# Kernel tuning notes

Hardware: AMD Instinct MI355X
Metric: run time of the kernel (lower is better)

## Reference

```python
import jax, jax.numpy as jnp
import numpy as np

N = 100000  # number of nodes
SELF_LOOP_W = 2.0  # improved=True in PyG GCNConv


def gcn_conv(x, edge_index, W, b):
    # x: [N, Fin], edge_index: [2, E] (row=src, col=dst), W: [Fin, Fout], b: [Fout]
    src, dst = edge_index[0], edge_index[1]
    h = x @ W  # [N, Fout]
    # degree with improved self-loops (weight 2.0)
    ones = jnp.ones(src.shape, dtype=h.dtype)
    deg = jax.ops.segment_sum(ones, dst, num_segments=N) + SELF_LOOP_W
    dinv = jnp.where(deg > 0, jax.lax.rsqrt(deg), 0.0)
    norm = dinv[src] * dinv[dst]  # [E]
    agg = jax.ops.segment_sum(h[src] * norm[:, None], dst, num_segments=N)
    # self-loop contribution: weight 2.0, norm = dinv_i * 2 * dinv_i
    agg = agg + h * (SELF_LOOP_W * dinv * dinv)[:, None]
    return agg + b


def setup_inputs() -> dict:
    key = jax.random.key(0)
    ks = jax.random.split(key, 6)
    x = jax.random.normal(ks[0], (N, 64), dtype=jnp.float32)
    edge_index = jax.random.randint(ks[1], (2, 1600000), 0, N, dtype=jnp.int64)
    W1 = jax.random.normal(ks[2], (64, 64), dtype=jnp.float32) * 0.1
    b1 = jax.random.normal(ks[3], (64,), dtype=jnp.float32) * 0.1
    W2 = jax.random.normal(ks[4], (64, 32), dtype=jnp.float32) * 0.1
    b2 = jax.random.normal(ks[5], (32,), dtype=jnp.float32) * 0.1
    return {"x": x, "edge_index": edge_index, "W1": W1, "b1": b1, "W2": W2, "b2": b2}


def reference(x, edge_index, W1, b1, W2, b2):
    h1 = jax.nn.relu(gcn_conv(x, edge_index, W1, b1))
    feature_map = h1
    out = gcn_conv(h1, edge_index, W2, b2)
    return (out, feature_map)
```

## Files before the change

### kernel.cpp

```cpp
#include <hip/hip_runtime.h>

#define N_NODES 100000
#define E_EDGES 1600000

#define BSHIFT 7
#define BSIZE 128
#define NBUCK ((N_NODES + BSIZE - 1) / BSIZE)
#define STAGE_TPB 512
#define STAGE_EPT 8
#define STAGE_CHUNK (STAGE_TPB * STAGE_EPT)
#define NREP 2
#define BUCKET_CAP 4096
#define CSR_STRIDE (BUCKET_CAP + 512)

typedef __attribute__((ext_vector_type(8))) short short8;
typedef __attribute__((ext_vector_type(4))) float float4v;
typedef __attribute__((ext_vector_type(2))) float float2v;
typedef __attribute__((ext_vector_type(4))) int int4v;
typedef __attribute__((ext_vector_type(4))) unsigned uint4v;

__device__ inline unsigned short f2bf(float f) {
    union { float f; unsigned u; } t; t.f = f;
    unsigned r = (t.u + 0x7fffu + ((t.u >> 16) & 1u)) >> 16;
    return (unsigned short)r;
}
__device__ inline float bf2f(unsigned short h) {
    union { unsigned u; float f; } t; t.u = ((unsigned)h) << 16; return t.f;
}
__device__ inline unsigned pack_bf16x2(float a, float b) {
    return (unsigned)f2bf(a) | ((unsigned)f2bf(b) << 16);
}
__device__ inline float bf_lo(unsigned u) { union { unsigned u; float f; } t; t.u = u << 16; return t.f; }
__device__ inline float bf_hi(unsigned u) { union { unsigned u; float f; } t; t.u = u & 0xffff0000u; return t.f; }

__device__ inline float2v bfpair(unsigned u) {
    float2v r;
    r[0] = bf_lo(u);
    r[1] = bf_hi(u);
    return r;
}
__device__ inline float2v pk_add(float2v a, float2v b) {
    float2v d;
    asm("v_pk_add_f32 %0, %1, %2" : "=v"(d) : "v"(a), "v"(b));
    return d;
}

__global__ void cursor_init_kernel(int* __restrict__ gcursor,
                                   unsigned* __restrict__ HS1, unsigned* __restrict__ HS2) {
    int b = blockIdx.x * blockDim.x + threadIdx.x;
    if (b < NBUCK) gcursor[b] = b * BUCKET_CAP;
    if (b < 32) HS1[(size_t)N_NODES * 32 + b] = 0u;
    if (b < 16) HS2[(size_t)N_NODES * 16 + b] = 0u;
}

__global__ void __launch_bounds__(STAGE_TPB) stage_kernel(
    const int* __restrict__ src, const int* __restrict__ dst,
    int* __restrict__ gcursor, unsigned* __restrict__ staged, int E) {
    __shared__ int hist[NREP][NBUCK];
    __shared__ int dbase[NBUCK];
    __shared__ int scanw[1024];
    __shared__ unsigned lrec[STAGE_CHUNK];
    __shared__ int laddr[STAGE_CHUNK];
    const int tid = threadIdx.x;
    const int rep = (tid >> 8) & (NREP - 1);
    const int e0 = blockIdx.x * STAGE_CHUNK;
    for (int i = tid; i < NREP * NBUCK; i += STAGE_TPB) ((int*)hist)[i] = 0;
    scanw[tid] = 0; scanw[tid + 512] = 0;
    __syncthreads();
    int d[STAGE_EPT], s[STAGE_EPT];
#pragma unroll
    for (int k = 0; k < STAGE_EPT / 4; ++k) {
        int e = e0 + (k * STAGE_TPB + tid) * 4;
        if (e < E) {
            int4v sv = __builtin_nontemporal_load((const int4v*)(src + e));
            int4v dv = __builtin_nontemporal_load((const int4v*)(dst + e));
#pragma unroll
            for (int i = 0; i < 4; ++i) {
                s[4 * k + i] = sv[i];
                d[4 * k + i] = dv[i];
                atomicAdd(&hist[rep][dv[i] >> BSHIFT], 1);
            }
        } else {
#pragma unroll
            for (int i = 0; i < 4; ++i) d[4 * k + i] = -1;
        }
    }
    __syncthreads();
    for (int i = tid; i < NBUCK; i += STAGE_TPB) scanw[i] = hist[0][i] + hist[1][i];
    if (tid + 512 < NBUCK) scanw[tid + 512] = hist[0][tid + 512] + hist[1][tid + 512];
    __syncthreads();
    for (int off = 1; off < 1024; off <<= 1) {
        int v0 = (tid >= off) ? scanw[tid - off] : 0;
        int v1 = (tid + 512 >= off) ? scanw[tid + 512 - off] : 0;
        __syncthreads();
        scanw[tid] += v0;
        scanw[tid + 512] += v1;
        __syncthreads();
    }
    for (int i = tid; i < NBUCK; i += STAGE_TPB) {
        int h0 = hist[0][i], h1 = hist[1][i];
        int t = h0 + h1;
        int excl = scanw[i] - t;
        if (t > 0) {
            int g = atomicAdd(&gcursor[i], t);
            dbase[i] = g - excl;
        }
        hist[0][i] = excl;
        hist[1][i] = excl + h0;
    }
    __syncthreads();
#pragma unroll
    for (int k = 0; k < STAGE_EPT; ++k) {
        if (d[k] >= 0) {
            int b = d[k] >> BSHIFT;
            int slot = atomicAdd(&hist[rep][b], 1);
            lrec[slot] = (unsigned)s[k] | ((unsigned)(d[k] & (BSIZE - 1)) << 17);
            laddr[slot] = dbase[b] + slot;
        }
    }
    __syncthreads();
    const int total = min(STAGE_CHUNK, E - e0);
    for (int i = tid; i < total; i += STAGE_TPB) {
        int a = laddr[i];
        if ((unsigned)a < (unsigned)(NBUCK * BUCKET_CAP))
            staged[a] = lrec[i];
    }
}

__global__ void bucket_csr_kernel(const unsigned* __restrict__ staged,
                                  const int* __restrict__ gcursor,
                                  int4v* __restrict__ meta, float* __restrict__ dinv,
                                  int* __restrict__ csrc, int n) {
    __shared__ int ldeg[BSIZE];
    __shared__ int laex[BSIZE];
    __shared__ int lscan[BSIZE];
    __shared__ int lcnt[BSIZE];
    __shared__ int h2[32];
    __shared__ int c2[32];
    __shared__ unsigned lrec[BUCKET_CAP];
    __shared__ int lsrc[BUCKET_CAP + 512];
    __shared__ int ltot;
    const int b = blockIdx.x;
    const int node0 = b * BSIZE;
    const int nn = min(BSIZE, n - node0);
    const int tid = threadIdx.x;
    if (tid < BSIZE) { ldeg[tid] = 0; lcnt[tid] = 0; }
    if (tid < 32) { h2[tid] = 0; c2[tid] = 0; }
    __syncthreads();
    const int ebase = b * CSR_STRIDE;
    int ecnt = gcursor[b] - b * BUCKET_CAP;
    if (ecnt > BUCKET_CAP) ecnt = BUCKET_CAP;
    const int sbase = b * BUCKET_CAP;
    for (int i = tid; i < ecnt; i += 256) {
        unsigned r = staged[sbase + i];
        lrec[i] = r;
        atomicAdd(&ldeg[(r >> 17) & (BSIZE - 1)], 1);
    }
    __syncthreads();
    int mydeg = (tid < BSIZE) ? ldeg[tid] : 0;
    int adeg = (mydeg + 3) & ~3;
    if (tid < BSIZE) lscan[tid] = adeg;
    __syncthreads();
    for (int off = 1; off < BSIZE; off <<= 1) {
        int v = 0;
        if (tid < BSIZE && tid >= off) v = lscan[tid - off];
        __syncthreads();
        if (tid < BSIZE) lscan[tid] += v;
        __syncthreads();
    }
    const int bin = min(adeg >> 2, 31);
    float mydinv = 0.0f;
    if (tid < BSIZE) {
        int aex = lscan[tid] - adeg;
        laex[tid] = aex;
        if (tid == BSIZE - 1) ltot = lscan[tid];
        if (tid < nn) {
            mydinv = rsqrtf((float)mydeg + 2.0f);
            dinv[node0 + tid] = mydinv;
            for (int k = mydeg; k < adeg; ++k) lsrc[aex + k] = N_NODES;
            atomicAdd(&h2[bin], 1);
        }
    }
    __syncthreads();
    if (tid == 0) {
        int acc = 0;
        for (int k = 0; k < 32; ++k) { int v = h2[k]; h2[k] = acc; acc += v; }
    }
    __syncthreads();
    if (tid < nn) {
        int pos = h2[bin] + atomicAdd(&c2[bin], 1);
        union { float f; int i; } dv; dv.f = mydinv;
        meta[node0 + pos] = (int4v){ebase + laex[tid], mydeg, node0 + tid, dv.i};
    }
    for (int i = tid; i < ecnt; i += 256) {
        unsigned r = lrec[i];
        int dl = (int)((r >> 17) & (BSIZE - 1));
        int sv = (int)(r & 0x1FFFFu);
        int pos = laex[dl] + atomicAdd(&lcnt[dl], 1);
        if (pos < BUCKET_CAP + 512) lsrc[pos] = sv;
    }
    __syncthreads();
    const int tot = ltot;
    for (int i = tid; i < tot; i += 256)
        csrc[ebase + i] = lsrc[i];
}

template <int FOUT>
__global__ void __launch_bounds__(256) linear_mfma_kernel(
    const float* __restrict__ X, const float* __restrict__ W,
    const float* __restrict__ dinv, unsigned* __restrict__ HS, int n) {
    constexpr int NT = FOUT / 16;
    constexpr int ROWU = NT * 8;
    const int NTILES_M = n / 16;
    const int lane = threadIdx.x & 63;
    const int gwave = blockIdx.x * 4 + (threadIdx.x >> 6);
    const int nwaves = gridDim.x * 4;
    const int m = lane & 15;
    const int q = lane >> 4;

    short8 Bhi[2][NT], Blo[2][NT];
#pragma unroll
    for (int ks = 0; ks < 2; ++ks)
#pragma unroll
        for (int nt = 0; nt < NT; ++nt) {
            short8 bh, bl;
#pragma unroll
            for (int j = 0; j < 8; ++j) {
                int k = ks * 32 + q * 8 + j;
                float wv = W[k * FOUT + nt * 16 + m];
                unsigned short h = f2bf(wv);
                bh[j] = (short)h;
                bl[j] = (short)f2bf(wv - bf2f(h));
            }
            Bhi[ks][nt] = bh;
            Blo[ks][nt] = bl;
        }

    for (int tile = gwave; tile < NTILES_M; tile += nwaves) {
        const int row0 = tile * 16;
        float4v C[NT];
#pragma unroll
        for (int nt = 0; nt < NT; ++nt) C[nt] = (float4v){0.f, 0.f, 0.f, 0.f};
#pragma unroll
        for (int ks = 0; ks < 2; ++ks) {
            const float* xp = X + (size_t)(row0 + m) * 64 + ks * 32 + q * 8;
            float4v x0 = __builtin_nontemporal_load((const float4v*)xp);
            float4v x1 = __builtin_nontemporal_load((const float4v*)(xp + 4));
            short8 Ahi, Alo;
#pragma unroll
            for (int j = 0; j < 4; ++j) {
                unsigned short h0 = f2bf(x0[j]);
                Ahi[j] = (short)h0;
                Alo[j] = (short)f2bf(x0[j] - bf2f(h0));
                unsigned short h1 = f2bf(x1[j]);
                Ahi[4 + j] = (short)h1;
                Alo[4 + j] = (short)f2bf(x1[j] - bf2f(h1));
            }
#pragma unroll
            for (int nt = 0; nt < NT; ++nt) {
                C[nt] = __builtin_amdgcn_mfma_f32_16x16x32_bf16(Ahi, Bhi[ks][nt], C[nt], 0, 0, 0);
                C[nt] = __builtin_amdgcn_mfma_f32_16x16x32_bf16(Alo, Bhi[ks][nt], C[nt], 0, 0, 0);
                C[nt] = __builtin_amdgcn_mfma_f32_16x16x32_bf16(Ahi, Blo[ks][nt], C[nt], 0, 0, 0);
            }
        }
#pragma unroll
        for (int ch = 0; ch < NT / 2; ++ch) {
#pragma unroll
            for (int reg = 0; reg < 4; ++reg) {
                int r = row0 + q * 4 + reg;
                float di = dinv[r];
                unsigned u = pack_bf16x2(C[2 * ch][reg] * di, C[2 * ch + 1][reg] * di);
                __builtin_nontemporal_store(u, HS + (size_t)r * ROWU + ch * 16 + m);
            }
        }
    }
}

template <int ROWU, bool RELU>
__global__ void __launch_bounds__(256) gather_vec_kernel(
    const int4v* __restrict__ meta, const int* __restrict__ csrc,
    const unsigned* __restrict__ HS, const float* __restrict__ bias,
    float* __restrict__ OUT, int n) {
    constexpr int G = ROWU / 4;
    constexpr int NPB = 256 / G;
    constexpr int FOUT = ROWU * 2;
    const int gslot = blockIdx.x * NPB + (int)(threadIdx.x / G);
    const int t = threadIdx.x % G;
    if (gslot >= n) return;
    const int4v mi = meta[gslot];
    const int start = mi[0];
    const int deg = mi[1];
    const int node = mi[2];
    union { int i; float f; } dv; dv.i = mi[3];
    const float dd = dv.f;
    const int pend = start + ((deg + 3) & ~3);
    const unsigned* __restrict__ HSt = HS + 4 * t;
    const uint4v own = *(const uint4v*)(HS + (size_t)node * ROWU + 4 * t);
    float2v acc[4];
#pragma unroll
    for (int k = 0; k < 4; ++k) {
        float2v o = bfpair(own[k]);
        acc[k][0] = 2.0f * o[0];
        acc[k][1] = 2.0f * o[1];
    }
    int j = start;
    for (; j + 8 <= pend; j += 8) {
        int4v s0 = __builtin_nontemporal_load((const int4v*)(csrc + j));
        int4v s1 = __builtin_nontemporal_load((const int4v*)(csrc + j + 4));
        uint4v u0 = *(const uint4v*)(HSt + (size_t)s0[0] * ROWU);
        uint4v u1 = *(const uint4v*)(HSt + (size_t)s0[1] * ROWU);
        uint4v u2 = *(const uint4v*)(HSt + (size_t)s0[2] * ROWU);
        uint4v u3 = *(const uint4v*)(HSt + (size_t)s0[3] * ROWU);
        uint4v u4 = *(const uint4v*)(HSt + (size_t)s1[0] * ROWU);
        uint4v u5 = *(const uint4v*)(HSt + (size_t)s1[1] * ROWU);
        uint4v u6 = *(const uint4v*)(HSt + (size_t)s1[2] * ROWU);
        uint4v u7 = *(const uint4v*)(HSt + (size_t)s1[3] * ROWU);
#pragma unroll
        for (int k = 0; k < 4; ++k) {
            float2v p01 = pk_add(bfpair(u0[k]), bfpair(u1[k]));
            float2v p23 = pk_add(bfpair(u2[k]), bfpair(u3[k]));
            float2v p45 = pk_add(bfpair(u4[k]), bfpair(u5[k]));
            float2v p67 = pk_add(bfpair(u6[k]), bfpair(u7[k]));
            acc[k] = pk_add(acc[k], pk_add(pk_add(p01, p23), pk_add(p45, p67)));
        }
    }
    if (j < pend) {
        int4v s0 = __builtin_nontemporal_load((const int4v*)(csrc + j));
        uint4v u0 = *(const uint4v*)(HSt + (size_t)s0[0] * ROWU);
        uint4v u1 = *(const uint4v*)(HSt + (size_t)s0[1] * ROWU);
        uint4v u2 = *(const uint4v*)(HSt + (size_t)s0[2] * ROWU);
        uint4v u3 = *(const uint4v*)(HSt + (size_t)s0[3] * ROWU);
#pragma unroll
        for (int k = 0; k < 4; ++k) {
            float2v p01 = pk_add(bfpair(u0[k]), bfpair(u1[k]));
            float2v p23 = pk_add(bfpair(u2[k]), bfpair(u3[k]));
            acc[k] = pk_add(acc[k], pk_add(p01, p23));
        }
    }
    const int ch = t >> 2;
    const int c0 = (4 * t) & 15;
    const float4v blv = *(const float4v*)(bias + 32 * ch + c0);
    const float4v bhv = *(const float4v*)(bias + 32 * ch + 16 + c0);
    float4v olo, ohi;
#pragma unroll
    for (int k = 0; k < 4; ++k) {
        float o0 = acc[k][0] * dd + blv[k];
        float o1 = acc[k][1] * dd + bhv[k];
        if (RELU) { o0 = fmaxf(o0, 0.0f); o1 = fmaxf(o1, 0.0f); }
        olo[k] = o0;
        ohi[k] = o1;
    }
    float* op = OUT + (size_t)node * FOUT + 32 * ch + c0;
    __builtin_nontemporal_store(olo, (float4v*)op);
    __builtin_nontemporal_store(ohi, (float4v*)(op + 16));
}

extern "C" void kernel_launch(void* const* d_in, const int* in_sizes, int n_in,
                              void* d_out, int out_size, void* d_ws, size_t ws_size,
                              hipStream_t stream) {
    const float* x  = (const float*)d_in[0];
    const int*   ei = (const int*)d_in[1];
    const float* W1 = (const float*)d_in[2];
    const float* b1 = (const float*)d_in[3];
    const float* W2 = (const float*)d_in[4];
    const float* b2 = (const float*)d_in[5];

    const int* srcp = ei;
    const int* dstp = ei + E_EDGES;

    float* out = (float*)d_out;
    float* fm  = (float*)d_out + N_NODES * 32;

    char* w = (char*)d_ws;
    auto alloc = [&w](size_t bytes) -> void* {
        uintptr_t p = ((uintptr_t)w + 255) & ~(uintptr_t)255;
        w = (char*)(p + bytes);
        return (void*)p;
    };
    int*      gcursor  = (int*)alloc(sizeof(int) * NBUCK);
    int4v*    meta     = (int4v*)alloc(sizeof(int4v) * N_NODES);
    float*    dinv     = (float*)alloc(sizeof(float) * N_NODES);
    int*      csrc     = (int*)alloc(sizeof(int) * (size_t)NBUCK * CSR_STRIDE);
    unsigned* staged   = (unsigned*)alloc(sizeof(unsigned) * (size_t)NBUCK * BUCKET_CAP);
    unsigned* HS1      = (unsigned*)alloc(sizeof(unsigned) * (size_t)(N_NODES + 1) * 32);
    unsigned* HS2      = (unsigned*)alloc(sizeof(unsigned) * (size_t)(N_NODES + 1) * 16);

    cursor_init_kernel<<<(NBUCK + 255) / 256, 256, 0, stream>>>(gcursor, HS1, HS2);
    stage_kernel<<<(E_EDGES + STAGE_CHUNK - 1) / STAGE_CHUNK, STAGE_TPB, 0, stream>>>(
        srcp, dstp, gcursor, staged, E_EDGES);
    bucket_csr_kernel<<<NBUCK, 256, 0, stream>>>(staged, gcursor, meta, dinv, csrc, N_NODES);

    linear_mfma_kernel<64><<<512, 256, 0, stream>>>(x, W1, dinv, HS1, N_NODES);
    gather_vec_kernel<32, true><<<(N_NODES + 31) / 32, 256, 0, stream>>>(
        meta, csrc, HS1, b1, fm, N_NODES);

    linear_mfma_kernel<32><<<512, 256, 0, stream>>>(fm, W2, dinv, HS2, N_NODES);
    gather_vec_kernel<16, false><<<(N_NODES + 63) / 64, 256, 0, stream>>>(
        meta, csrc, HS2, b2, out, N_NODES);
}
```

Before: 197.8 us.

## Run first-layer GEMM concurrently with edge staging and fuse dinv scaling into CSR build

Extra blocks are appended to the edge staging kernel that compute the unscaled x@W1 product into a new fp32 buffer P, so the GEMM overlaps with the atomic-heavy bucketing work. The bucket CSR kernel then reads P, scales each row by its freshly computed dinv, packs to bf16 and writes HS1, which removes the separate first linear kernel launch. The cost is an extra round trip of a 100000x64 fp32 intermediate through memory and more shared/register pressure in the merged kernel, and the GEMM blocks share the stage kernel's large LDS footprint, which may limit occupancy.

```diff
diff --git a/kernel.cpp b/kernel.cpp
--- a/kernel.cpp
+++ b/kernel.cpp
@@ -9,6 +9,8 @@
 #define STAGE_TPB 512
 #define STAGE_EPT 8
 #define STAGE_CHUNK (STAGE_TPB * STAGE_EPT)
+#define NSTAGE ((E_EDGES + STAGE_CHUNK - 1) / STAGE_CHUNK)
+#define NGEMM 121
 #define NREP 2
 #define BUCKET_CAP 4096
 #define CSR_STRIDE (BUCKET_CAP + 512)
@@ -53,88 +55,152 @@
     if (b < 16) HS2[(size_t)N_NODES * 16 + b] = 0u;
 }
 
-__global__ void __launch_bounds__(STAGE_TPB) stage_kernel(
+__global__ void __launch_bounds__(STAGE_TPB) stage_gemm_kernel(
     const int* __restrict__ src, const int* __restrict__ dst,
-    int* __restrict__ gcursor, unsigned* __restrict__ staged, int E) {
-    __shared__ int hist[NREP][NBUCK];
-    __shared__ int dbase[NBUCK];
-    __shared__ int scanw[1024];
-    __shared__ unsigned lrec[STAGE_CHUNK];
-    __shared__ int laddr[STAGE_CHUNK];
+    int* __restrict__ gcursor, unsigned* __restrict__ staged,
+    const float* __restrict__ X, const float* __restrict__ W,
+    float* __restrict__ P, int E, int n) {
     const int tid = threadIdx.x;
-    const int rep = (tid >> 8) & (NREP - 1);
-    const int e0 = blockIdx.x * STAGE_CHUNK;
-    for (int i = tid; i < NREP * NBUCK; i += STAGE_TPB) ((int*)hist)[i] = 0;
-    scanw[tid] = 0; scanw[tid + 512] = 0;
-    __syncthreads();
-    int d[STAGE_EPT], s[STAGE_EPT];
-#pragma unroll
-    for (int k = 0; k < STAGE_EPT / 4; ++k) {
-        int e = e0 + (k * STAGE_TPB + tid) * 4;
-        if (e < E) {
-            int4v sv = __builtin_nontemporal_load((const int4v*)(src + e));
-            int4v dv = __builtin_nontemporal_load((const int4v*)(dst + e));
-#pragma unroll
-            for (int i = 0; i < 4; ++i) {
-                s[4 * k + i] = sv[i];
-                d[4 * k + i] = dv[i];
-                atomicAdd(&hist[rep][dv[i] >> BSHIFT], 1);
-            }
-        } else {
-#pragma unroll
-            for (int i = 0; i < 4; ++i) d[4 * k + i] = -1;
-        }
-    }
-    __syncthreads();
-    for (int i = tid; i < NBUCK; i += STAGE_TPB) scanw[i] = hist[0][i] + hist[1][i];
-    if (tid + 512 < NBUCK) scanw[tid + 512] = hist[0][tid + 512] + hist[1][tid + 512];
-    __syncthreads();
-    for (int off = 1; off < 1024; off <<= 1) {
-        int v0 = (tid >= off) ? scanw[tid - off] : 0;
-        int v1 = (tid + 512 >= off) ? scanw[tid + 512 - off] : 0;
-        __syncthreads();
-        scanw[tid] += v0;
-        scanw[tid + 512] += v1;
-        __syncthreads();
-    }
-    for (int i = tid; i < NBUCK; i += STAGE_TPB) {
-        int h0 = hist[0][i], h1 = hist[1][i];
-        int t = h0 + h1;
-        int excl = scanw[i] - t;
-        if (t > 0) {
-            int g = atomicAdd(&gcursor[i], t);
-            dbase[i] = g - excl;
-        }
-        hist[0][i] = excl;
-        hist[1][i] = excl + h0;
-    }
-    __syncthreads();
-#pragma unroll
-    for (int k = 0; k < STAGE_EPT; ++k) {
-        if (d[k] >= 0) {
-            int b = d[k] >> BSHIFT;
-            int slot = atomicAdd(&hist[rep][b], 1);
-            lrec[slot] = (unsigned)s[k] | ((unsigned)(d[k] & (BSIZE - 1)) << 17);
-            laddr[slot] = dbase[b] + slot;
-        }
-    }
-    __syncthreads();
-    const int total = min(STAGE_CHUNK, E - e0);
-    for (int i = tid; i < total; i += STAGE_TPB) {
-        int a = laddr[i];
-        if ((unsigned)a < (unsigned)(NBUCK * BUCKET_CAP))
-            staged[a] = lrec[i];
+    if (blockIdx.x < NSTAGE) {
+        __shared__ int hist[NREP][NBUCK];
+        __shared__ int dbase[NBUCK];
+        __shared__ int scanw[1024];
+        __shared__ unsigned lrec[STAGE_CHUNK];
+        __shared__ int laddr[STAGE_CHUNK];
+        const int rep = (tid >> 8) & (NREP - 1);
+        const int e0 = blockIdx.x * STAGE_CHUNK;
+        for (int i = tid; i < NREP * NBUCK; i += STAGE_TPB) ((int*)hist)[i] = 0;
+        scanw[tid] = 0; scanw[tid + 512] = 0;
+        __syncthreads();
+        int d[STAGE_EPT], s[STAGE_EPT];
+#pragma unroll
+        for (int k = 0; k < STAGE_EPT / 4; ++k) {
+            int e = e0 + (k * STAGE_TPB + tid) * 4;
+            if (e < E) {
+                int4v sv = __builtin_nontemporal_load((const int4v*)(src + e));
+                int4v dv = __builtin_nontemporal_load((const int4v*)(dst + e));
+#pragma unroll
+                for (int i = 0; i < 4; ++i) {
+                    s[4 * k + i] = sv[i];
+                    d[4 * k + i] = dv[i];
+                    atomicAdd(&hist[rep][dv[i] >> BSHIFT], 1);
+                }
+            } else {
+#pragma unroll
+                for (int i = 0; i < 4; ++i) d[4 * k + i] = -1;
+            }
+        }
+        __syncthreads();
+        for (int i = tid; i < NBUCK; i += STAGE_TPB) scanw[i] = hist[0][i] + hist[1][i];
+        if (tid + 512 < NBUCK) scanw[tid + 512] = hist[0][tid + 512] + hist[1][tid + 512];
+        __syncthreads();
+        for (int off = 1; off < 1024; off <<= 1) {
+            int v0 = (tid >= off) ? scanw[tid - off] : 0;
+            int v1 = (tid + 512 >= off) ? scanw[tid + 512 - off] : 0;
+            __syncthreads();
+            scanw[tid] += v0;
+            scanw[tid + 512] += v1;
+            __syncthreads();
+        }
+        for (int i = tid; i < NBUCK; i += STAGE_TPB) {
+            int h0 = hist[0][i], h1 = hist[1][i];
+            int t = h0 + h1;
+            int excl = scanw[i] - t;
+            if (t > 0) {
+                int g = atomicAdd(&gcursor[i], t);
+                dbase[i] = g - excl;
+            }
+            hist[0][i] = excl;
+            hist[1][i] = excl + h0;
+        }
+        __syncthreads();
+#pragma unroll
+        for (int k = 0; k < STAGE_EPT; ++k) {
+            if (d[k] >= 0) {
+                int b = d[k] >> BSHIFT;
+                int slot = atomicAdd(&hist[rep][b], 1);
+                lrec[slot] = (unsigned)s[k] | ((unsigned)(d[k] & (BSIZE - 1)) << 17);
+                laddr[slot] = dbase[b] + slot;
+            }
+        }
+        __syncthreads();
+        const int total = min(STAGE_CHUNK, E - e0);
+        for (int i = tid; i < total; i += STAGE_TPB) {
+            int a = laddr[i];
+            if ((unsigned)a < (unsigned)(NBUCK * BUCKET_CAP))
+                staged[a] = lrec[i];
+        }
+    } else {
+        constexpr int NT = 4;
+        const int NTILES_M = n / 16;
+        const int lane = tid & 63;
+        const int gwave = (blockIdx.x - NSTAGE) * 8 + (tid >> 6);
+        const int nwaves = NGEMM * 8;
+        const int m = lane & 15;
+        const int q = lane >> 4;
+        short8 Bhi[2][NT], Blo[2][NT];
+#pragma unroll
+        for (int ks = 0; ks < 2; ++ks)
+#pragma unroll
+            for (int nt = 0; nt < NT; ++nt) {
+                short8 bh, bl;
+#pragma unroll
+                for (int j = 0; j < 8; ++j) {
+                    int k = ks * 32 + q * 8 + j;
+                    float wv = W[k * 64 + nt * 16 + m];
+                    unsigned short h = f2bf(wv);
+                    bh[j] = (short)h;
+                    bl[j] = (short)f2bf(wv - bf2f(h));
+                }
+                Bhi[ks][nt] = bh;
+                Blo[ks][nt] = bl;
+            }
+        for (int tile = gwave; tile < NTILES_M; tile += nwaves) {
+            const int row0 = tile * 16;
+            float4v C[NT];
+#pragma unroll
+            for (int nt = 0; nt < NT; ++nt) C[nt] = (float4v){0.f, 0.f, 0.f, 0.f};
+#pragma unroll
+            for (int ks = 0; ks < 2; ++ks) {
+                const float* xp = X + (size_t)(row0 + m) * 64 + ks * 32 + q * 8;
+                float4v x0 = __builtin_nontemporal_load((const float4v*)xp);
+                float4v x1 = __builtin_nontemporal_load((const float4v*)(xp + 4));
+                short8 Ahi, Alo;
+#pragma unroll
+                for (int j = 0; j < 4; ++j) {
+                    unsigned short h0 = f2bf(x0[j]);
+                    Ahi[j] = (short)h0;
+                    Alo[j] = (short)f2bf(x0[j] - bf2f(h0));
+                    unsigned short h1 = f2bf(x1[j]);
+                    Ahi[4 + j] = (short)h1;
+                    Alo[4 + j] = (short)f2bf(x1[j] - bf2f(h1));
+                }
+#pragma unroll
+                for (int nt = 0; nt < NT; ++nt) {
+                    C[nt] = __builtin_amdgcn_mfma_f32_16x16x32_bf16(Ahi, Bhi[ks][nt], C[nt], 0, 0, 0);
+                    C[nt] = __builtin_amdgcn_mfma_f32_16x16x32_bf16(Alo, Bhi[ks][nt], C[nt], 0, 0, 0);
+                    C[nt] = __builtin_amdgcn_mfma_f32_16x16x32_bf16(Ahi, Blo[ks][nt], C[nt], 0, 0, 0);
+                }
+            }
+#pragma unroll
+            for (int nt = 0; nt < NT; ++nt)
+#pragma unroll
+                for (int reg = 0; reg < 4; ++reg)
+                    P[(size_t)(row0 + q * 4 + reg) * 64 + nt * 16 + m] = C[nt][reg];
+        }
     }
 }
 
 __global__ void bucket_csr_kernel(const unsigned* __restrict__ staged,
                                   const int* __restrict__ gcursor,
+                                  const float* __restrict__ P,
                                   int4v* __restrict__ meta, float* __restrict__ dinv,
-                                  int* __restrict__ csrc, int n) {
+                                  int* __restrict__ csrc, unsigned* __restrict__ HS1, int n) {
     __shared__ int ldeg[BSIZE];
     __shared__ int laex[BSIZE];
     __shared__ int lscan[BSIZE];
     __shared__ int lcnt[BSIZE];
+    __shared__ float ldv[BSIZE];
     __shared__ int h2[32];
     __shared__ int c2[32];
     __shared__ unsigned lrec[BUCKET_CAP];
@@ -177,6 +243,7 @@
         if (tid < nn) {
             mydinv = rsqrtf((float)mydeg + 2.0f);
             dinv[node0 + tid] = mydinv;
+            ldv[tid] = mydinv;
             for (int k = mydeg; k < adeg; ++k) lsrc[aex + k] = N_NODES;
             atomicAdd(&h2[bin], 1);
         }
@@ -203,6 +270,22 @@
     const int tot = ltot;
     for (int i = tid; i < tot; i += 256)
         csrc[ebase + i] = lsrc[i];
+    for (int i = tid; i < nn * 2; i += 256) {
+        const int nloc = i >> 1, h = i & 1;
+        const int node = node0 + nloc;
+        const float di = ldv[nloc];
+        const float* pr = P + (size_t)node * 64 + 32 * h;
+        unsigned* op = HS1 + (size_t)node * 32 + 16 * h;
+#pragma unroll
+        for (int c0 = 0; c0 < 16; c0 += 4) {
+            float4v lo = *(const float4v*)(pr + c0);
+            float4v hi = *(const float4v*)(pr + 16 + c0);
+            uint4v u;
+#pragma unroll
+            for (int k = 0; k < 4; ++k) u[k] = pack_bf16x2(lo[k] * di, hi[k] * di);
+            __builtin_nontemporal_store(u, (uint4v*)(op + c0));
+        }
+    }
 }
 
 template <int FOUT>
@@ -380,17 +463,18 @@
     int*      gcursor  = (int*)alloc(sizeof(int) * NBUCK);
     int4v*    meta     = (int4v*)alloc(sizeof(int4v) * N_NODES);
     float*    dinv     = (float*)alloc(sizeof(float) * N_NODES);
+    float*    P        = (float*)alloc(sizeof(float) * (size_t)N_NODES * 64);
     int*      csrc     = (int*)alloc(sizeof(int) * (size_t)NBUCK * CSR_STRIDE);
     unsigned* staged   = (unsigned*)alloc(sizeof(unsigned) * (size_t)NBUCK * BUCKET_CAP);
     unsigned* HS1      = (unsigned*)alloc(sizeof(unsigned) * (size_t)(N_NODES + 1) * 32);
     unsigned* HS2      = (unsigned*)alloc(sizeof(unsigned) * (size_t)(N_NODES + 1) * 16);
 
     cursor_init_kernel<<<(NBUCK + 255) / 256, 256, 0, stream>>>(gcursor, HS1, HS2);
-    stage_kernel<<<(E_EDGES + STAGE_CHUNK - 1) / STAGE_CHUNK, STAGE_TPB, 0, stream>>>(
-        srcp, dstp, gcursor, staged, E_EDGES);
-    bucket_csr_kernel<<<NBUCK, 256, 0, stream>>>(staged, gcursor, meta, dinv, csrc, N_NODES);
-
-    linear_mfma_kernel<64><<<512, 256, 0, stream>>>(x, W1, dinv, HS1, N_NODES);
+    stage_gemm_kernel<<<NSTAGE + NGEMM, STAGE_TPB, 0, stream>>>(
+        srcp, dstp, gcursor, staged, x, W1, P, E_EDGES, N_NODES);
+    bucket_csr_kernel<<<NBUCK, 256, 0, stream>>>(staged, gcursor, P, meta, dinv, csrc,
+                                                 HS1, N_NODES);
+
     gather_vec_kernel<32, true><<<(N_NODES + 31) / 32, 256, 0, stream>>>(
         meta, csrc, HS1, b1, fm, N_NODES);
 
```

New measurement: 216.4 us. 9.4% more time.
